# Kernel tuning notes

Measured on AMD Instinct MI355X. Metric: run time of the kernel, lower is better.

## Reference

```python
import jax, jax.numpy as jnp
import numpy as np

HID = 512
NB = 20
N = 65536
EPS = 1e-5


def layer_norm(x, g, b):
    m = jnp.mean(x, axis=-1, keepdims=True)
    v = jnp.mean(jnp.square(x - m), axis=-1, keepdims=True)
    return (x - m) * jax.lax.rsqrt(v + EPS) * g + b


def setup_inputs() -> dict:
    key = jax.random.key(0)
    ks = jax.random.split(key, 8)
    s = 0.02
    return {
        "x": jax.random.normal(ks[0], (N, 2), dtype=jnp.float32),
        "in_w": jax.random.normal(ks[1], (2, HID), dtype=jnp.float32) * s,
        "in_b": jnp.zeros((HID,), jnp.float32),
        "ln1_g": jnp.ones((NB, HID), jnp.float32),
        "ln1_b": jnp.zeros((NB, HID), jnp.float32),
        "fc1_w": jax.random.normal(ks[2], (NB, HID, HID), dtype=jnp.float32) * s,
        "fc1_b": jnp.zeros((NB, HID), jnp.float32),
        "ln2_g": jnp.ones((NB, HID), jnp.float32),
        "ln2_b": jnp.zeros((NB, HID), jnp.float32),
        "fc2_w": jax.random.normal(ks[3], (NB, HID, HID), dtype=jnp.float32) * s,
        "fc2_b": jnp.zeros((NB, HID), jnp.float32),
        "out_ln_g": jnp.ones((HID,), jnp.float32),
        "out_ln_b": jnp.zeros((HID,), jnp.float32),
        "out_w": jax.random.normal(ks[4], (HID, 1), dtype=jnp.float32) * s,
        "out_b": jnp.zeros((1,), jnp.float32),
    }


def reference(x, in_w, in_b, ln1_g, ln1_b, fc1_w, fc1_b, ln2_g, ln2_b,
              fc2_w, fc2_b, out_ln_g, out_ln_b, out_w, out_b):
    # in_proj + SiLU: [N,2] @ [2,HID]
    h = jax.nn.silu(x @ in_w + in_b)

    def block(h, p):
        g1, b1, w1, c1, g2, b2, w2, c2 = p
        t = jax.nn.silu(layer_norm(h, g1, b1) @ w1 + c1)
        t = layer_norm(t, g2, b2) @ w2 + c2
        return h + t, None

    h, _ = jax.lax.scan(block, h, (ln1_g, ln1_b, fc1_w, fc1_b,
                                   ln2_g, ln2_b, fc2_w, fc2_b))
    h = jax.nn.silu(layer_norm(h, out_ln_g, out_ln_b))
    return h @ out_w + out_b  # [N, 1]
```

## Files before the change

### kernel.cpp

```cpp
#include <hip/hip_runtime.h>
#include <hip/hip_bf16.h>


typedef float  fvec4 __attribute__((ext_vector_type(4)));
typedef __bf16 bvec8 __attribute__((ext_vector_type(8)));

#define HN_STRIDE 520
#define WCHUNK    16384
#define SMEM_BYTES (64*HN_STRIDE*2 + 64*8)
#define WPK_USHORTS ((size_t)20*2*16*WCHUNK)

__device__ __forceinline__ unsigned int f2bf(float v) {
    unsigned int u = __float_as_uint(v);
    return (u + 0x7fffu + ((u >> 16) & 1u)) >> 16;
}
__device__ __forceinline__ unsigned int pkbf(float a, float b) {
    __hip_bfloat162 t = __float22bfloat162_rn(make_float2(a, b));
    unsigned int r;
    __builtin_memcpy(&r, &t, 4);
    return r;
}
__device__ __forceinline__ float silu_f(float v) {
    return v * (1.0f / (1.0f + __expf(-v)));
}

__global__ __launch_bounds__(256) void pack_weights(
        const float* __restrict__ w1, const float* __restrict__ w2,
        const float* __restrict__ g1, const float* __restrict__ g2,
        unsigned short* __restrict__ pk) {
    int tid = blockIdx.x * 256 + threadIdx.x;
    int l  = tid & 63;
    int f  = tid >> 6;
    int t  = f & 1;
    int kc = (f >> 1) & 15;
    int w  = (f >> 5) & 15;
    int g  = (f >> 9) & 1;
    int b  = f >> 10;
    const float* src = g ? w2 : w1;
    const float* gs  = (g ? g2 : g1) + b * 512;
    int k0 = kc * 32 + (l >> 4) * 8;
    int n  = w * 32 + (l & 15) * 2 + t;
    const float* s = src + ((size_t)b * 512 + k0) * 512 + n;
    unsigned int r[4];
#pragma unroll
    for (int j = 0; j < 4; ++j) {
        float ga = gs[k0 + 2 * j];
        float gb = gs[k0 + 2 * j + 1];
        unsigned int lo = f2bf(ga * s[(size_t)(2*j) * 512]);
        unsigned int hi = f2bf(gb * s[(size_t)(2*j + 1) * 512]);
        r[j] = lo | (hi << 16);
    }
    *(uint4*)(pk + (size_t)tid * 8) = make_uint4(r[0], r[1], r[2], r[3]);
}

__global__ __launch_bounds__(512) void make_uv(
        const float* __restrict__ w1, const float* __restrict__ w2,
        const float* __restrict__ g1, const float* __restrict__ bl1,
        const float* __restrict__ cb1,
        const float* __restrict__ g2, const float* __restrict__ bl2,
        const float* __restrict__ cb2,
        float* __restrict__ uv) {
    int b = blockIdx.x >> 1, slot = blockIdx.x & 1, n = threadIdx.x;
    const float* W  = (slot ? w2 : w1) + (size_t)b * 512 * 512;
    const float* g  = (slot ? g2 : g1) + b * 512;
    const float* bl = (slot ? bl2 : bl1) + b * 512;
    const float* cb = (slot ? cb2 : cb1) + b * 512;
    float u = 0.f, v = 0.f;
    for (int j = 0; j < 512; ++j) {
        float wv = W[(size_t)j * 512 + n];
        u = fmaf(g[j], wv, u);
        v = fmaf(bl[j], wv, v);
    }
    uv[((b * 2 + slot) * 2 + 0) * 512 + n] = u;
    uv[((b * 2 + slot) * 2 + 1) * 512 + n] = v + cb[n];
}

__device__ __forceinline__ void acc_u32(unsigned int u, float& s, float& ss) {
    float lo = __uint_as_float(u << 16);
    float hi = __uint_as_float(u & 0xFFFF0000u);
    s += lo + hi;
    ss = __builtin_fmaf(lo, lo, ss);
    ss = __builtin_fmaf(hi, hi, ss);
}

__device__ __forceinline__ void gemm_red(
        fvec4 acc[4][2], const unsigned short* hn,
        const unsigned short* __restrict__ wp, uint4 pre0, uint4 pre1,
        float2* mv, int l, int c, int q, int tid) {
    const uint4* wp4 = (const uint4*)wp;
    const int r = tid >> 4, j = tid & 15;
    float s = 0.f, ss = 0.f;
#pragma unroll
    for (int kc = 0; kc < 16; ++kc) {
        bvec8 a[4], b0, b1;
#pragma unroll
        for (int rb = 0; rb < 4; ++rb)
            a[rb] = *(const bvec8*)(hn + (rb * 16 + c) * HN_STRIDE + kc * 32 + q * 8);
        if (kc == 0) {
            __builtin_memcpy(&b0, &pre0, 16);
            __builtin_memcpy(&b1, &pre1, 16);
        } else {
            uint4 r0 = wp4[(kc * 2 + 0) * 64 + l];
            uint4 r1 = wp4[(kc * 2 + 1) * 64 + l];
            __builtin_memcpy(&b0, &r0, 16);
            __builtin_memcpy(&b1, &r1, 16);
        }
        if (kc >= 4 && kc < 8) {
            uint4 pv = *(const uint4*)(hn + r * HN_STRIDE + (j + 16 * (kc - 4)) * 8);
            acc_u32(pv.x, s, ss); acc_u32(pv.y, s, ss);
            acc_u32(pv.z, s, ss); acc_u32(pv.w, s, ss);
        }
#pragma unroll
        for (int rb = 0; rb < 4; ++rb) {
            acc[rb][0] = __builtin_amdgcn_mfma_f32_16x16x32_bf16(a[rb], b0, acc[rb][0], 0, 0, 0);
            acc[rb][1] = __builtin_amdgcn_mfma_f32_16x16x32_bf16(a[rb], b1, acc[rb][1], 0, 0, 0);
        }
    }
    s += __shfl_xor(s, 1); ss += __shfl_xor(ss, 1);
    s += __shfl_xor(s, 2); ss += __shfl_xor(ss, 2);
    s += __shfl_xor(s, 4); ss += __shfl_xor(ss, 4);
    s += __shfl_xor(s, 8); ss += __shfl_xor(ss, 8);
    if (j == 0) {
        float mean = s * (1.f / 512.f);
        float var  = ss * (1.f / 512.f) - mean * mean;
        mv[r] = make_float2(mean, rsqrtf(var + 1e-5f));
    }
}

__device__ __forceinline__ void reduce_mv_hn(const unsigned short* hn,
                                             float2* mv, int tid) {
    int r = tid >> 4, j = tid & 15;
    float s = 0.f, ss = 0.f;
#pragma unroll
    for (int u = 0; u < 4; ++u) {
        uint4 pv = *(const uint4*)(hn + r * HN_STRIDE + (j + 16 * u) * 8);
        acc_u32(pv.x, s, ss); acc_u32(pv.y, s, ss);
        acc_u32(pv.z, s, ss); acc_u32(pv.w, s, ss);
    }
    s += __shfl_xor(s, 1); ss += __shfl_xor(ss, 1);
    s += __shfl_xor(s, 2); ss += __shfl_xor(ss, 2);
    s += __shfl_xor(s, 4); ss += __shfl_xor(ss, 4);
    s += __shfl_xor(s, 8); ss += __shfl_xor(ss, 8);
    if (j == 0) {
        float mean = s * (1.f / 512.f);
        float var  = ss * (1.f / 512.f) - mean * mean;
        mv[r] = make_float2(mean, rsqrtf(var + 1e-5f));
    }
}

__global__ __launch_bounds__(1024, 4) void mlp_fused(
        const float* __restrict__ x,
        const float* __restrict__ in_w,  const float* __restrict__ in_b,
        const float* __restrict__ out_ln_g, const float* __restrict__ out_ln_b,
        const float* __restrict__ out_w, const float* __restrict__ out_b,
        const unsigned short* __restrict__ wpk,
        const float* __restrict__ uv,
        float* __restrict__ out) {
    extern __shared__ char smem[];
    unsigned short* hn = (unsigned short*)smem;
    float* hnf = (float*)smem;
    float2* mv = (float2*)(smem + 64 * HN_STRIDE * 2);

    const int tid = threadIdx.x;
    const int w = tid >> 6;
    const int l = tid & 63, c = l & 15, q = l >> 4;
    const int colbase = w * 32 + c * 2;
    const int row0 = blockIdx.x * 64;

    float h[4][4][2];

    {
        float2 iw0 = *(const float2*)(in_w + colbase);
        float2 iw1 = *(const float2*)(in_w + 512 + colbase);
        float2 ib  = *(const float2*)(in_b + colbase);
#pragma unroll
        for (int rb = 0; rb < 4; ++rb)
#pragma unroll
            for (int i = 0; i < 4; ++i) {
                int row = rb * 16 + q * 4 + i;
                float2 xv = *(const float2*)(x + (size_t)(row0 + row) * 2);
                h[rb][i][0] = silu_f(xv.x * iw0.x + xv.y * iw1.x + ib.x);
                h[rb][i][1] = silu_f(xv.x * iw0.y + xv.y * iw1.y + ib.y);
            }
    }

    for (int b = 0; b < 20; ++b) {
        const unsigned short* wp1 = wpk + ((size_t)(b * 2 + 0) * 16 + w) * WCHUNK;
        const unsigned short* wp2 = wpk + ((size_t)(b * 2 + 1) * 16 + w) * WCHUNK;
        float2 u1  = *(const float2*)(uv + ((b * 2 + 0) * 2 + 0) * 512 + colbase);
        float2 vc1 = *(const float2*)(uv + ((b * 2 + 0) * 2 + 1) * 512 + colbase);
        float2 u2  = *(const float2*)(uv + ((b * 2 + 1) * 2 + 0) * 512 + colbase);
        float2 vc2 = *(const float2*)(uv + ((b * 2 + 1) * 2 + 1) * 512 + colbase);

        uint4 pre0 = ((const uint4*)wp1)[l];
        uint4 pre1 = ((const uint4*)wp1)[64 + l];
#pragma unroll
        for (int rb = 0; rb < 4; ++rb)
#pragma unroll
            for (int i = 0; i < 4; ++i) {
                int row = rb * 16 + q * 4 + i;
                *(unsigned int*)(hn + row * HN_STRIDE + colbase) =
                    pkbf(h[rb][i][0], h[rb][i][1]);
            }
        __syncthreads();

        fvec4 acc[4][2];
#pragma unroll
        for (int rb = 0; rb < 4; ++rb)
#pragma unroll
            for (int t = 0; t < 2; ++t) acc[rb][t] = (fvec4){0.f, 0.f, 0.f, 0.f};
        gemm_red(acc, hn, wp1, pre0, pre1, mv, l, c, q, tid);
        __syncthreads();

        pre0 = ((const uint4*)wp2)[l];
        pre1 = ((const uint4*)wp2)[64 + l];
#pragma unroll
        for (int rb = 0; rb < 4; ++rb)
#pragma unroll
            for (int i = 0; i < 4; ++i) {
                int row = rb * 16 + q * 4 + i;
                float2 m = mv[row];
                float minv = -m.x * m.y;
                float t0 = silu_f(__builtin_fmaf(acc[rb][0][i], m.y,
                                  __builtin_fmaf(minv, u1.x, vc1.x)));
                float t1 = silu_f(__builtin_fmaf(acc[rb][1][i], m.y,
                                  __builtin_fmaf(minv, u1.y, vc1.y)));
                *(unsigned int*)(hn + row * HN_STRIDE + colbase) = pkbf(t0, t1);
            }
        __syncthreads();

#pragma unroll
        for (int rb = 0; rb < 4; ++rb)
#pragma unroll
            for (int t = 0; t < 2; ++t) acc[rb][t] = (fvec4){0.f, 0.f, 0.f, 0.f};
        gemm_red(acc, hn, wp2, pre0, pre1, mv, l, c, q, tid);
        __syncthreads();

#pragma unroll
        for (int rb = 0; rb < 4; ++rb)
#pragma unroll
            for (int i = 0; i < 4; ++i) {
                int row = rb * 16 + q * 4 + i;
                float2 m = mv[row];
                float minv = -m.x * m.y;
                h[rb][i][0] = __builtin_fmaf(acc[rb][0][i], m.y,
                    h[rb][i][0] + __builtin_fmaf(minv, u2.x, vc2.x));
                h[rb][i][1] = __builtin_fmaf(acc[rb][1][i], m.y,
                    h[rb][i][1] + __builtin_fmaf(minv, u2.y, vc2.y));
            }
    }

#pragma unroll
    for (int rb = 0; rb < 4; ++rb)
#pragma unroll
        for (int i = 0; i < 4; ++i) {
            int row = rb * 16 + q * 4 + i;
            *(unsigned int*)(hn + row * HN_STRIDE + colbase) =
                pkbf(h[rb][i][0], h[rb][i][1]);
        }
    __syncthreads();
    reduce_mv_hn(hn, mv, tid);
    __syncthreads();
    {
        float2 og = *(const float2*)(out_ln_g + colbase);
        float2 ob = *(const float2*)(out_ln_b + colbase);
        float2 ow = *(const float2*)(out_w + colbase);
        const int pcol = w * 16 + c;
#pragma unroll
    for (int rb = 0; rb < 4; ++rb)
#pragma unroll
            for (int i = 0; i < 4; ++i) {
                int row = rb * 16 + q * 4 + i;
                float2 m = mv[row];
                float v0 = (h[rb][i][0] - m.x) * m.y * og.x + ob.x;
                float v1 = (h[rb][i][1] - m.x) * m.y * og.y + ob.y;
                hnf[pcol * 65 + row] = silu_f(v0) * ow.x + silu_f(v1) * ow.y;
            }
    }
    __syncthreads();
    {
        int r = tid >> 4, j = tid & 15;
        float s = 0.f;
#pragma unroll
        for (int u = 0; u < 16; ++u)
            s += hnf[(j + 16 * u) * 65 + r];
        s += __shfl_xor(s, 1);
        s += __shfl_xor(s, 2);
        s += __shfl_xor(s, 4);
        s += __shfl_xor(s, 8);
        if (j == 0) out[row0 + r] = s + out_b[0];
    }
}

extern "C" void kernel_launch(void* const* d_in, const int* in_sizes, int n_in,
                              void* d_out, int out_size, void* d_ws, size_t ws_size,
                              hipStream_t stream) {
    const float* x        = (const float*)d_in[0];
    const float* in_w     = (const float*)d_in[1];
    const float* in_b     = (const float*)d_in[2];
    const float* ln1_g    = (const float*)d_in[3];
    const float* ln1_b    = (const float*)d_in[4];
    const float* fc1_w    = (const float*)d_in[5];
    const float* fc1_b    = (const float*)d_in[6];
    const float* ln2_g    = (const float*)d_in[7];
    const float* ln2_b    = (const float*)d_in[8];
    const float* fc2_w    = (const float*)d_in[9];
    const float* fc2_b    = (const float*)d_in[10];
    const float* out_ln_g = (const float*)d_in[11];
    const float* out_ln_b = (const float*)d_in[12];
    const float* out_w    = (const float*)d_in[13];
    const float* out_b    = (const float*)d_in[14];
    float* out = (float*)d_out;
    unsigned short* wpk = (unsigned short*)d_ws;
    float* uv = (float*)((char*)d_ws + WPK_USHORTS * 2);

    (void)hipFuncSetAttribute((const void*)mlp_fused,
                              hipFuncAttributeMaxDynamicSharedMemorySize, SMEM_BYTES);

    pack_weights<<<5120, 256, 0, stream>>>(fc1_w, fc2_w, ln1_g, ln2_g, wpk);
    make_uv<<<40, 512, 0, stream>>>(fc1_w, fc2_w, ln1_g, ln1_b, fc1_b,
                                    ln2_g, ln2_b, fc2_b, uv);
    mlp_fused<<<1024, 1024, SMEM_BYTES, stream>>>(
        x, in_w, in_b, out_ln_g, out_ln_b, out_w, out_b, wpk, uv, out);
}
```

Measured before the change: 1.802 ms.

## Halve block to 8 waves with 64-column tiles, register-prefetch weights, rotate K order

Each wave now computes 64 output columns (4 MFMA N-tiles) instead of 32, so blocks shrink from 1024 to 512 threads and each A fragment read from LDS feeds twice as many MFMAs. The weight pack layout is changed to match. Weight fragments are double-buffered in registers so the next K-chunk's global load is issued before the current MFMAs run. The K-loop start is rotated per block to spread L2 access across weight chunks. The cost is roughly double the accumulator and h registers per thread, which may limit occupancy or cause spills.

```diff
diff --git a/kernel.cpp b/kernel.cpp
--- a/kernel.cpp
+++ b/kernel.cpp
@@ -6,9 +6,9 @@
 typedef __bf16 bvec8 __attribute__((ext_vector_type(8)));
 
 #define HN_STRIDE 520
-#define WCHUNK    16384
+#define WCHUNK    32768
 #define SMEM_BYTES (64*HN_STRIDE*2 + 64*8)
-#define WPK_USHORTS ((size_t)20*2*16*WCHUNK)
+#define WPK_USHORTS ((size_t)20*2*8*WCHUNK)
 
 __device__ __forceinline__ unsigned int f2bf(float v) {
     unsigned int u = __float_as_uint(v);
@@ -31,15 +31,15 @@
     int tid = blockIdx.x * 256 + threadIdx.x;
     int l  = tid & 63;
     int f  = tid >> 6;
-    int t  = f & 1;
-    int kc = (f >> 1) & 15;
-    int w  = (f >> 5) & 15;
+    int t  = f & 3;
+    int kc = (f >> 2) & 15;
+    int w  = (f >> 6) & 7;
     int g  = (f >> 9) & 1;
     int b  = f >> 10;
     const float* src = g ? w2 : w1;
     const float* gs  = (g ? g2 : g1) + b * 512;
     int k0 = kc * 32 + (l >> 4) * 8;
-    int n  = w * 32 + (l & 15) * 2 + t;
+    int n  = w * 64 + (l & 15) * 4 + t;
     const float* s = src + ((size_t)b * 512 + k0) * 512 + n;
     unsigned int r[4];
 #pragma unroll
@@ -84,42 +84,48 @@
 }
 
 __device__ __forceinline__ void gemm_red(
-        fvec4 acc[4][2], const unsigned short* hn,
-        const unsigned short* __restrict__ wp, uint4 pre0, uint4 pre1,
-        float2* mv, int l, int c, int q, int tid) {
+        fvec4 acc[4][4], const unsigned short* hn,
+        const unsigned short* __restrict__ wp, const uint4* pre,
+        float2* mv, int l, int c, int q, int tid, int rot) {
     const uint4* wp4 = (const uint4*)wp;
-    const int r = tid >> 4, j = tid & 15;
+    const int r = tid >> 3, j = tid & 7;
     float s = 0.f, ss = 0.f;
-#pragma unroll
-    for (int kc = 0; kc < 16; ++kc) {
-        bvec8 a[4], b0, b1;
+    uint4 bcur[4] = {pre[0], pre[1], pre[2], pre[3]};
+#pragma unroll
+    for (int it = 0; it < 16; ++it) {
+        const int kc = (it + rot) & 15;
+        uint4 bnxt[4];
+        if (it < 15) {
+            const int kn = (kc + 1) & 15;
+#pragma unroll
+            for (int t = 0; t < 4; ++t) bnxt[t] = wp4[(kn * 4 + t) * 64 + l];
+        }
+        bvec8 a[4];
 #pragma unroll
         for (int rb = 0; rb < 4; ++rb)
             a[rb] = *(const bvec8*)(hn + (rb * 16 + c) * HN_STRIDE + kc * 32 + q * 8);
-        if (kc == 0) {
-            __builtin_memcpy(&b0, &pre0, 16);
-            __builtin_memcpy(&b1, &pre1, 16);
-        } else {
-            uint4 r0 = wp4[(kc * 2 + 0) * 64 + l];
-            uint4 r1 = wp4[(kc * 2 + 1) * 64 + l];
-            __builtin_memcpy(&b0, &r0, 16);
-            __builtin_memcpy(&b1, &r1, 16);
-        }
-        if (kc >= 4 && kc < 8) {
-            uint4 pv = *(const uint4*)(hn + r * HN_STRIDE + (j + 16 * (kc - 4)) * 8);
+        if (it >= 4 && it < 12) {
+            uint4 pv = *(const uint4*)(hn + r * HN_STRIDE + (j + 8 * (it - 4)) * 8);
             acc_u32(pv.x, s, ss); acc_u32(pv.y, s, ss);
             acc_u32(pv.z, s, ss); acc_u32(pv.w, s, ss);
         }
 #pragma unroll
         for (int rb = 0; rb < 4; ++rb) {
-            acc[rb][0] = __builtin_amdgcn_mfma_f32_16x16x32_bf16(a[rb], b0, acc[rb][0], 0, 0, 0);
-            acc[rb][1] = __builtin_amdgcn_mfma_f32_16x16x32_bf16(a[rb], b1, acc[rb][1], 0, 0, 0);
+#pragma unroll
+            for (int t = 0; t < 4; ++t) {
+                bvec8 bb;
+                __builtin_memcpy(&bb, &bcur[t], 16);
+                acc[rb][t] = __builtin_amdgcn_mfma_f32_16x16x32_bf16(a[rb], bb, acc[rb][t], 0, 0, 0);
+            }
+        }
+        if (it < 15) {
+#pragma unroll
+            for (int t = 0; t < 4; ++t) bcur[t] = bnxt[t];
         }
     }
     s += __shfl_xor(s, 1); ss += __shfl_xor(ss, 1);
     s += __shfl_xor(s, 2); ss += __shfl_xor(ss, 2);
     s += __shfl_xor(s, 4); ss += __shfl_xor(ss, 4);
-    s += __shfl_xor(s, 8); ss += __shfl_xor(ss, 8);
     if (j == 0) {
         float mean = s * (1.f / 512.f);
         float var  = ss * (1.f / 512.f) - mean * mean;
@@ -129,18 +135,17 @@
 
 __device__ __forceinline__ void reduce_mv_hn(const unsigned short* hn,
                                              float2* mv, int tid) {
-    int r = tid >> 4, j = tid & 15;
+    int r = tid >> 3, j = tid & 7;
     float s = 0.f, ss = 0.f;
 #pragma unroll
-    for (int u = 0; u < 4; ++u) {
-        uint4 pv = *(const uint4*)(hn + r * HN_STRIDE + (j + 16 * u) * 8);
+    for (int u = 0; u < 8; ++u) {
+        uint4 pv = *(const uint4*)(hn + r * HN_STRIDE + (j + 8 * u) * 8);
         acc_u32(pv.x, s, ss); acc_u32(pv.y, s, ss);
         acc_u32(pv.z, s, ss); acc_u32(pv.w, s, ss);
     }
     s += __shfl_xor(s, 1); ss += __shfl_xor(ss, 1);
     s += __shfl_xor(s, 2); ss += __shfl_xor(ss, 2);
     s += __shfl_xor(s, 4); ss += __shfl_xor(ss, 4);
-    s += __shfl_xor(s, 8); ss += __shfl_xor(ss, 8);
     if (j == 0) {
         float mean = s * (1.f / 512.f);
         float var  = ss * (1.f / 512.f) - mean * mean;
@@ -148,7 +153,7 @@
     }
 }
 
-__global__ __launch_bounds__(1024, 4) void mlp_fused(
+__global__ __launch_bounds__(512, 2) void mlp_fused(
         const float* __restrict__ x,
         const float* __restrict__ in_w,  const float* __restrict__ in_b,
         const float* __restrict__ out_ln_g, const float* __restrict__ out_ln_b,
@@ -164,76 +169,81 @@
     const int tid = threadIdx.x;
     const int w = tid >> 6;
     const int l = tid & 63, c = l & 15, q = l >> 4;
-    const int colbase = w * 32 + c * 2;
+    const int colbase = w * 64 + c * 4;
     const int row0 = blockIdx.x * 64;
-
-    float h[4][4][2];
+    const int rot = blockIdx.x & 15;
+
+    float h[4][4][4];
 
     {
-        float2 iw0 = *(const float2*)(in_w + colbase);
-        float2 iw1 = *(const float2*)(in_w + 512 + colbase);
-        float2 ib  = *(const float2*)(in_b + colbase);
+        fvec4 iw0 = *(const fvec4*)(in_w + colbase);
+        fvec4 iw1 = *(const fvec4*)(in_w + 512 + colbase);
+        fvec4 ib  = *(const fvec4*)(in_b + colbase);
 #pragma unroll
         for (int rb = 0; rb < 4; ++rb)
 #pragma unroll
             for (int i = 0; i < 4; ++i) {
                 int row = rb * 16 + q * 4 + i;
                 float2 xv = *(const float2*)(x + (size_t)(row0 + row) * 2);
-                h[rb][i][0] = silu_f(xv.x * iw0.x + xv.y * iw1.x + ib.x);
-                h[rb][i][1] = silu_f(xv.x * iw0.y + xv.y * iw1.y + ib.y);
+#pragma unroll
+                for (int t = 0; t < 4; ++t)
+                    h[rb][i][t] = silu_f(xv.x * iw0[t] + xv.y * iw1[t] + ib[t]);
+                *(uint2*)(hn + row * HN_STRIDE + colbase) =
+                    make_uint2(pkbf(h[rb][i][0], h[rb][i][1]),
+                               pkbf(h[rb][i][2], h[rb][i][3]));
             }
     }
 
     for (int b = 0; b < 20; ++b) {
-        const unsigned short* wp1 = wpk + ((size_t)(b * 2 + 0) * 16 + w) * WCHUNK;
-        const unsigned short* wp2 = wpk + ((size_t)(b * 2 + 1) * 16 + w) * WCHUNK;
-        float2 u1  = *(const float2*)(uv + ((b * 2 + 0) * 2 + 0) * 512 + colbase);
-        float2 vc1 = *(const float2*)(uv + ((b * 2 + 0) * 2 + 1) * 512 + colbase);
-        float2 u2  = *(const float2*)(uv + ((b * 2 + 1) * 2 + 0) * 512 + colbase);
-        float2 vc2 = *(const float2*)(uv + ((b * 2 + 1) * 2 + 1) * 512 + colbase);
-
-        uint4 pre0 = ((const uint4*)wp1)[l];
-        uint4 pre1 = ((const uint4*)wp1)[64 + l];
-#pragma unroll
-        for (int rb = 0; rb < 4; ++rb)
-#pragma unroll
-            for (int i = 0; i < 4; ++i) {
-                int row = rb * 16 + q * 4 + i;
-                *(unsigned int*)(hn + row * HN_STRIDE + colbase) =
-                    pkbf(h[rb][i][0], h[rb][i][1]);
-            }
+        const unsigned short* wp1 = wpk + (size_t)(b * 16 + w) * WCHUNK;
+        const unsigned short* wp2 = wpk + (size_t)(b * 16 + 8 + w) * WCHUNK;
+        fvec4 u1  = *(const fvec4*)(uv + ((b * 2 + 0) * 2 + 0) * 512 + colbase);
+        fvec4 vc1 = *(const fvec4*)(uv + ((b * 2 + 0) * 2 + 1) * 512 + colbase);
+        fvec4 u2  = *(const fvec4*)(uv + ((b * 2 + 1) * 2 + 0) * 512 + colbase);
+        fvec4 vc2 = *(const fvec4*)(uv + ((b * 2 + 1) * 2 + 1) * 512 + colbase);
+
+        uint4 pre[4];
+#pragma unroll
+        for (int t = 0; t < 4; ++t)
+            pre[t] = ((const uint4*)wp1)[(rot * 4 + t) * 64 + l];
         __syncthreads();
 
-        fvec4 acc[4][2];
-#pragma unroll
-        for (int rb = 0; rb < 4; ++rb)
-#pragma unroll
-            for (int t = 0; t < 2; ++t) acc[rb][t] = (fvec4){0.f, 0.f, 0.f, 0.f};
-        gemm_red(acc, hn, wp1, pre0, pre1, mv, l, c, q, tid);
+        fvec4 acc[4][4];
+#pragma unroll
+        for (int rb = 0; rb < 4; ++rb)
+#pragma unroll
+            for (int t = 0; t < 4; ++t) acc[rb][t] = (fvec4){0.f, 0.f, 0.f, 0.f};
+        gemm_red(acc, hn, wp1, pre, mv, l, c, q, tid, rot);
         __syncthreads();
 
-        pre0 = ((const uint4*)wp2)[l];
-        pre1 = ((const uint4*)wp2)[64 + l];
+#pragma unroll
+        for (int t = 0; t < 4; ++t)
+            pre[t] = ((const uint4*)wp2)[(rot * 4 + t) * 64 + l];
 #pragma unroll
         for (int rb = 0; rb < 4; ++rb)
 #pragma unroll
             for (int i = 0; i < 4; ++i) {
                 int row = rb * 16 + q * 4 + i;
                 float2 m = mv[row];
-                float minv = -m.x * m.y;
-                float t0 = silu_f(__builtin_fmaf(acc[rb][0][i], m.y,
-                                  __builtin_fmaf(minv, u1.x, vc1.x)));
-                float t1 = silu_f(__builtin_fmaf(acc[rb][1][i], m.y,
-                                  __builtin_fmaf(minv, u1.y, vc1.y)));
-                *(unsigned int*)(hn + row * HN_STRIDE + colbase) = pkbf(t0, t1);
+                float inv = m.y, minv = -m.x * m.y;
+                float t0 = silu_f(__builtin_fmaf(acc[rb][0][i], inv,
+                                  __builtin_fmaf(minv, u1[0], vc1[0])));
+                float t1 = silu_f(__builtin_fmaf(acc[rb][1][i], inv,
+                                  __builtin_fmaf(minv, u1[1], vc1[1])));
+                float t2 = silu_f(__builtin_fmaf(acc[rb][2][i], inv,
+                                  __builtin_fmaf(minv, u1[2], vc1[2])));
+                float t3 = silu_f(__builtin_fmaf(acc[rb][3][i], inv,
+                                  __builtin_fmaf(minv, u1[3], vc1[3])));
+                *(uint2*)(hn + row * HN_STRIDE + colbase) =
+                    make_uint2(pkbf(t0, t1), pkbf(t2, t3));
             }
         __syncthreads();
 
 #pragma unroll
         for (int rb = 0; rb < 4; ++rb)
 #pragma unroll
-            for (int t = 0; t < 2; ++t) acc[rb][t] = (fvec4){0.f, 0.f, 0.f, 0.f};
-        gemm_red(acc, hn, wp2, pre0, pre1, mv, l, c, q, tid);
+            for (int t = 0; t < 4; ++t) acc[rb][t] = (fvec4){0.f, 0.f, 0.f, 0.f};
+        gemm_red(acc, hn, wp2, pre, mv, l, c, q, tid, rot);
         __syncthreads();
 
 #pragma unroll
@@ -242,52 +252,50 @@
             for (int i = 0; i < 4; ++i) {
                 int row = rb * 16 + q * 4 + i;
                 float2 m = mv[row];
-                float minv = -m.x * m.y;
-                h[rb][i][0] = __builtin_fmaf(acc[rb][0][i], m.y,
-                    h[rb][i][0] + __builtin_fmaf(minv, u2.x, vc2.x));
-                h[rb][i][1] = __builtin_fmaf(acc[rb][1][i], m.y,
-                    h[rb][i][1] + __builtin_fmaf(minv, u2.y, vc2.y));
-            }
-    }
-
-#pragma unroll
-    for (int rb = 0; rb < 4; ++rb)
-#pragma unroll
-        for (int i = 0; i < 4; ++i) {
-            int row = rb * 16 + q * 4 + i;
-            *(unsigned int*)(hn + row * HN_STRIDE + colbase) =
-                pkbf(h[rb][i][0], h[rb][i][1]);
-        }
+                float inv = m.y, minv = -m.x * m.y;
+#pragma unroll
+                for (int t = 0; t < 4; ++t)
+                    h[rb][i][t] = __builtin_fmaf(acc[rb][t][i], inv,
+                        h[rb][i][t] + __builtin_fmaf(minv, u2[t], vc2[t]));
+                *(uint2*)(hn + row * HN_STRIDE + colbase) =
+                    make_uint2(pkbf(h[rb][i][0], h[rb][i][1]),
+                               pkbf(h[rb][i][2], h[rb][i][3]));
+            }
+    }
+
     __syncthreads();
     reduce_mv_hn(hn, mv, tid);
     __syncthreads();
     {
-        float2 og = *(const float2*)(out_ln_g + colbase);
-        float2 ob = *(const float2*)(out_ln_b + colbase);
-        float2 ow = *(const float2*)(out_w + colbase);
+        fvec4 og = *(const fvec4*)(out_ln_g + colbase);
+        fvec4 ob = *(const fvec4*)(out_ln_b + colbase);
+        fvec4 ow = *(const fvec4*)(out_w + colbase);
         const int pcol = w * 16 + c;
 #pragma unroll
-    for (int rb = 0; rb < 4; ++rb)
+        for (int rb = 0; rb < 4; ++rb)
 #pragma unroll
             for (int i = 0; i < 4; ++i) {
                 int row = rb * 16 + q * 4 + i;
                 float2 m = mv[row];
-                float v0 = (h[rb][i][0] - m.x) * m.y * og.x + ob.x;
-                float v1 = (h[rb][i][1] - m.x) * m.y * og.y + ob.y;
-                hnf[pcol * 65 + row] = silu_f(v0) * ow.x + silu_f(v1) * ow.y;
+                float sacc = 0.f;
+#pragma unroll
+                for (int t = 0; t < 4; ++t) {
+                    float v = (h[rb][i][t] - m.x) * m.y * og[t] + ob[t];
+                    sacc += silu_f(v) * ow[t];
+                }
+                hnf[pcol * 65 + row] = sacc;
             }
     }
     __syncthreads();
     {
-        int r = tid >> 4, j = tid & 15;
+        int r = tid >> 3, j = tid & 7;
         float s = 0.f;
 #pragma unroll
         for (int u = 0; u < 16; ++u)
-            s += hnf[(j + 16 * u) * 65 + r];
+            s += hnf[(j + 8 * u) * 65 + r];
         s += __shfl_xor(s, 1);
         s += __shfl_xor(s, 2);
         s += __shfl_xor(s, 4);
-        s += __shfl_xor(s, 8);
         if (j == 0) out[row0 + r] = s + out_b[0];
     }
 }
@@ -320,6 +328,6 @@
     pack_weights<<<5120, 256, 0, stream>>>(fc1_w, fc2_w, ln1_g, ln2_g, wpk);
     make_uv<<<40, 512, 0, stream>>>(fc1_w, fc2_w, ln1_g, ln1_b, fc1_b,
                                     ln2_g, ln2_b, fc2_b, uv);
-    mlp_fused<<<1024, 1024, SMEM_BYTES, stream>>>(
+    mlp_fused<<<1024, 512, SMEM_BYTES, stream>>>(
         x, in_w, in_b, out_ln_g, out_ln_b, out_w, out_b, wpk, uv, out);
 }
```

Measured after the change: 1.992 ms. +10.5%, slower.

## Stream weight tiles into LDS via async global_load_lds triple buffering

Applied to the files above, without the earlier changes.

Replaces direct per-lane global loads of packed weight fragments inside the GEMM loop with async global-to-LDS DMA into a three-slot ring buffer per wave. The loads are issued three units ahead, with explicit vmcnt waits. The next GEMM's first tiles are prefetched during the elementwise epilogues. The goal is to hide weight-load latency behind MFMA work. It adds 48KB of LDS per block, which may lower occupancy, and relies on hand-counted vmcnt ordering that other global loads could disturb.

```diff
diff --git a/kernel.cpp b/kernel.cpp
--- a/kernel.cpp
+++ b/kernel.cpp
@@ -7,7 +7,9 @@
 
 #define HN_STRIDE 520
 #define WCHUNK    16384
-#define SMEM_BYTES (64*HN_STRIDE*2 + 64*8)
+#define LDSB_OFF  (64*HN_STRIDE*2 + 64*8)
+#define SLOT_B    16384
+#define SMEM_BYTES (LDSB_OFF + 3*SLOT_B)
 #define WPK_USHORTS ((size_t)20*2*16*WCHUNK)
 
 __device__ __forceinline__ unsigned int f2bf(float v) {
@@ -22,6 +24,21 @@
 }
 __device__ __forceinline__ float silu_f(float v) {
     return v * (1.0f / (1.0f + __expf(-v)));
+}
+
+typedef const __attribute__((address_space(1))) void* as1p;
+typedef __attribute__((address_space(3))) void*       as3p;
+__device__ __forceinline__ void dma_b(const unsigned short* wp, char* ldsB,
+                                      int u, int w, int l) {
+    const void* g = (const void*)(wp + (size_t)u * 512 + l * 8);
+    void* d = (void*)(ldsB + (u % 3) * SLOT_B + w * 1024);
+    __builtin_amdgcn_global_load_lds((as1p)g, (as3p)d, 16, 0, 0);
+}
+__device__ __forceinline__ void dma_prologue(const unsigned short* wp,
+                                             char* ldsB, int w, int l) {
+    dma_b(wp, ldsB, 0, w, l);
+    dma_b(wp, ldsB, 1, w, l);
+    dma_b(wp, ldsB, 2, w, l);
 }
 
 __global__ __launch_bounds__(256) void pack_weights(
@@ -84,36 +101,38 @@
 }
 
 __device__ __forceinline__ void gemm_red(
-        fvec4 acc[4][2], const unsigned short* hn,
-        const unsigned short* __restrict__ wp, uint4 pre0, uint4 pre1,
-        float2* mv, int l, int c, int q, int tid) {
-    const uint4* wp4 = (const uint4*)wp;
+        fvec4 acc[4][2], const unsigned short* hn, char* ldsB,
+        const unsigned short* __restrict__ wp,
+        float2* mv, int l, int c, int q, int tid, int w) {
     const int r = tid >> 4, j = tid & 15;
     float s = 0.f, ss = 0.f;
 #pragma unroll
     for (int kc = 0; kc < 16; ++kc) {
-        bvec8 a[4], b0, b1;
+        bvec8 a[4];
 #pragma unroll
         for (int rb = 0; rb < 4; ++rb)
             a[rb] = *(const bvec8*)(hn + (rb * 16 + c) * HN_STRIDE + kc * 32 + q * 8);
-        if (kc == 0) {
-            __builtin_memcpy(&b0, &pre0, 16);
-            __builtin_memcpy(&b1, &pre1, 16);
-        } else {
-            uint4 r0 = wp4[(kc * 2 + 0) * 64 + l];
-            uint4 r1 = wp4[(kc * 2 + 1) * 64 + l];
-            __builtin_memcpy(&b0, &r0, 16);
-            __builtin_memcpy(&b1, &r1, 16);
-        }
         if (kc >= 4 && kc < 8) {
             uint4 pv = *(const uint4*)(hn + r * HN_STRIDE + (j + 16 * (kc - 4)) * 8);
             acc_u32(pv.x, s, ss); acc_u32(pv.y, s, ss);
             acc_u32(pv.z, s, ss); acc_u32(pv.w, s, ss);
         }
 #pragma unroll
-        for (int rb = 0; rb < 4; ++rb) {
-            acc[rb][0] = __builtin_amdgcn_mfma_f32_16x16x32_bf16(a[rb], b0, acc[rb][0], 0, 0, 0);
-            acc[rb][1] = __builtin_amdgcn_mfma_f32_16x16x32_bf16(a[rb], b1, acc[rb][1], 0, 0, 0);
+        for (int t = 0; t < 2; ++t) {
+            const int u = kc * 2 + t;
+            if (u <= 29) {
+                asm volatile("s_waitcnt vmcnt(2)" ::: "memory");
+            } else if (u == 30) {
+                asm volatile("s_waitcnt vmcnt(1)" ::: "memory");
+            } else {
+                asm volatile("s_waitcnt vmcnt(0)" ::: "memory");
+            }
+            bvec8 bb = *((const bvec8*)(ldsB + (u % 3) * SLOT_B + (size_t)w * 1024) + l);
+#pragma unroll
+            for (int rb = 0; rb < 4; ++rb)
+                acc[rb][t] = __builtin_amdgcn_mfma_f32_16x16x32_bf16(a[rb], bb, acc[rb][t], 0, 0, 0);
+            __builtin_amdgcn_sched_barrier(0x387);
+            if (u + 3 < 32) dma_b(wp, ldsB, u + 3, w, l);
         }
     }
     s += __shfl_xor(s, 1); ss += __shfl_xor(ss, 1);
@@ -160,6 +179,7 @@
     unsigned short* hn = (unsigned short*)smem;
     float* hnf = (float*)smem;
     float2* mv = (float2*)(smem + 64 * HN_STRIDE * 2);
+    char* ldsB = smem + LDSB_OFF;
 
     const int tid = threadIdx.x;
     const int w = tid >> 6;
@@ -169,7 +189,10 @@
 
     float h[4][4][2];
 
+    const unsigned short* wp1 = wpk + (size_t)w * WCHUNK;
+
     {
+        dma_prologue(wp1, ldsB, w, l);
         float2 iw0 = *(const float2*)(in_w + colbase);
         float2 iw1 = *(const float2*)(in_w + 512 + colbase);
         float2 ib  = *(const float2*)(in_b + colbase);
@@ -185,15 +208,13 @@
     }
 
     for (int b = 0; b < 20; ++b) {
-        const unsigned short* wp1 = wpk + ((size_t)(b * 2 + 0) * 16 + w) * WCHUNK;
+        wp1 = wpk + ((size_t)(b * 2 + 0) * 16 + w) * WCHUNK;
         const unsigned short* wp2 = wpk + ((size_t)(b * 2 + 1) * 16 + w) * WCHUNK;
         float2 u1  = *(const float2*)(uv + ((b * 2 + 0) * 2 + 0) * 512 + colbase);
         float2 vc1 = *(const float2*)(uv + ((b * 2 + 0) * 2 + 1) * 512 + colbase);
         float2 u2  = *(const float2*)(uv + ((b * 2 + 1) * 2 + 0) * 512 + colbase);
         float2 vc2 = *(const float2*)(uv + ((b * 2 + 1) * 2 + 1) * 512 + colbase);
 
-        uint4 pre0 = ((const uint4*)wp1)[l];
-        uint4 pre1 = ((const uint4*)wp1)[64 + l];
 #pragma unroll
         for (int rb = 0; rb < 4; ++rb)
 #pragma unroll
@@ -209,11 +230,10 @@
         for (int rb = 0; rb < 4; ++rb)
 #pragma unroll
             for (int t = 0; t < 2; ++t) acc[rb][t] = (fvec4){0.f, 0.f, 0.f, 0.f};
-        gemm_red(acc, hn, wp1, pre0, pre1, mv, l, c, q, tid);
+        gemm_red(acc, hn, ldsB, wp1, mv, l, c, q, tid, w);
         __syncthreads();
 
-        pre0 = ((const uint4*)wp2)[l];
-        pre1 = ((const uint4*)wp2)[64 + l];
+        dma_prologue(wp2, ldsB, w, l);
 #pragma unroll
         for (int rb = 0; rb < 4; ++rb)
 #pragma unroll
@@ -233,9 +253,12 @@
         for (int rb = 0; rb < 4; ++rb)
 #pragma unroll
             for (int t = 0; t < 2; ++t) acc[rb][t] = (fvec4){0.f, 0.f, 0.f, 0.f};
-        gemm_red(acc, hn, wp2, pre0, pre1, mv, l, c, q, tid);
+        gemm_red(acc, hn, ldsB, wp2, mv, l, c, q, tid, w);
         __syncthreads();
 
+        int bn = (b < 19) ? b + 1 : 19;
+        const unsigned short* wp1n = wpk + ((size_t)(bn * 2) * 16 + w) * WCHUNK;
+        dma_prologue(wp1n, ldsB, w, l);
 #pragma unroll
         for (int rb = 0; rb < 4; ++rb)
 #pragma unroll
```

Result: slower. 1.883 ms (+4.5%).
